# Optimization experiments

Measured on AMD Instinct MI355X. Metric: run time of the kernel, lower is better.

## Reference

```python
import jax, jax.numpy as jnp
import numpy as np

# ViT-Base config
C, H, W = 3, 224, 224
NP = 14            # n_patches per side
PS = 16            # patch size (H // NP)
IN_D = C * PS * PS # 768
D = 768            # hidden_d
NH = 12            # n_heads
DH = D // NH       # 64
L = 12             # n_blocks
MLP = 4 * D        # mlp_ratio * hidden_d
OUT = 1000         # out_d
B = 64             # batch
S = NP * NP + 1    # 197 tokens (cls + patches)
EPS = 1e-5


def _pos_embed(seq_len, d):
    # get_positional_embeddings: sin on even dims, cos on odd dims
    i = jnp.arange(seq_len, dtype=jnp.float32)[:, None]
    j = jnp.arange(d, dtype=jnp.float32)[None, :]
    angle = i / jnp.power(10000.0, (j - j % 2) / d)
    return jnp.where(j % 2 == 0, jnp.sin(angle), jnp.cos(angle))


def _ln(x, g, b):
    m = x.mean(-1, keepdims=True)
    v = ((x - m) ** 2).mean(-1, keepdims=True)
    return (x - m) * jax.lax.rsqrt(v + EPS) * g + b


def _attn(x, qkv_w, qkv_b, out_w, out_b):
    n, s, _ = x.shape
    qkv = (x @ qkv_w + qkv_b).reshape(n, s, NH, 3, DH)  # matches torch chunk layout
    q, k, v = qkv[..., 0, :], qkv[..., 1, :], qkv[..., 2, :]
    scores = jnp.einsum('bqhd,bkhd->bhqk', q, k) / (DH ** 0.5)
    w = jax.nn.softmax(scores, axis=-1)
    o = jnp.einsum('bhqk,bkhd->bqhd', w, v).reshape(n, s, D)
    return o @ out_w + out_b


def setup_inputs() -> dict:
    key = jax.random.key(0)
    ks = jax.random.split(key, 16)
    sd = 0.02
    return {
        'images': jax.random.normal(ks[0], (B, C, H, W), jnp.float32),
        'lm_w': jax.random.normal(ks[1], (IN_D, D), jnp.float32) * sd,
        'lm_b': jnp.zeros((D,), jnp.float32),
        'cls_tok': jax.random.uniform(ks[2], (1, D), jnp.float32),
        'ln1_g': jnp.ones((L, D), jnp.float32),
        'ln1_b': jnp.zeros((L, D), jnp.float32),
        'qkv_w': jax.random.normal(ks[3], (L, D, 3 * D), jnp.float32) * sd,
        'qkv_b': jnp.zeros((L, 3 * D), jnp.float32),
        'out_w': jax.random.normal(ks[4], (L, D, D), jnp.float32) * sd,
        'out_b': jnp.zeros((L, D), jnp.float32),
        'ln2_g': jnp.ones((L, D), jnp.float32),
        'ln2_b': jnp.zeros((L, D), jnp.float32),
        'mlp1_w': jax.random.normal(ks[5], (L, D, MLP), jnp.float32) * sd,
        'mlp1_b': jnp.zeros((L, MLP), jnp.float32),
        'mlp2_w': jax.random.normal(ks[6], (L, MLP, D), jnp.float32) * sd,
        'mlp2_b': jnp.zeros((L, D), jnp.float32),
        'head_w': jax.random.normal(ks[7], (D, OUT), jnp.float32) * sd,
        'head_b': jnp.zeros((OUT,), jnp.float32),
    }


def reference(images, lm_w, lm_b, cls_tok, ln1_g, ln1_b, qkv_w, qkv_b,
              out_w, out_b, ln2_g, ln2_b, mlp1_w, mlp1_b, mlp2_w, mlp2_b,
              head_w, head_b):
    n = images.shape[0]
    # patchify: (N,C,H,W) -> (N, NP*NP, C*PS*PS), per-patch flatten order (C, ph, pw)
    p = images.reshape(n, C, NP, PS, NP, PS).transpose(0, 2, 4, 1, 3, 5)
    p = p.reshape(n, NP * NP, IN_D)
    tok = p @ lm_w + lm_b                                   # (N, 196, D)
    cls = jnp.broadcast_to(cls_tok, (n, 1, D))
    x = jnp.concatenate([cls, tok], axis=1) + _pos_embed(S, D)
    for l in range(L):
        x = x + _attn(_ln(x, ln1_g[l], ln1_b[l]), qkv_w[l], qkv_b[l], out_w[l], out_b[l])
        h = _ln(x, ln2_g[l], ln2_b[l])
        x = x + (jax.nn.gelu(h @ mlp1_w[l] + mlp1_b[l], approximate=False) @ mlp2_w[l] + mlp2_b[l])
    return jax.nn.softmax(x[:, 0] @ head_w + head_b, axis=-1)
```

## Files before the change

kernel.cpp:

```cpp
#include <hip/hip_runtime.h>
#include <hip/hip_bf16.h>
#include <math.h>

#define WS_B 64
#define WS_S 197
#define WS_D 768
#define WS_NH 12
#define WS_L 12
#define WS_MLP 3072
#define WS_OUT 1000
#define WS_IND 768
#define WS_NPAT 196
#define SP 208
#define JP 224

typedef __attribute__((ext_vector_type(8))) short bf16x8;
typedef __attribute__((ext_vector_type(4))) float f32x4;

static __device__ __forceinline__ float bf2f(short s) {
    unsigned u = ((unsigned)(unsigned short)s) << 16;
    return __builtin_bit_cast(float, u);
}
static __device__ __forceinline__ short f2bf(float f) {
    unsigned u = __builtin_bit_cast(unsigned, f);
    u = (u + 0x7FFF + ((u >> 16) & 1)) >> 16;
    return (short)u;
}

static __device__ __forceinline__ int xcd_remap(int wg, int nwg) {
    int q = nwg >> 3, r = nwg & 7;
    int xcd = wg & 7, idx = wg >> 3;
    return (xcd < r ? xcd * (q + 1) : r * (q + 1) + (xcd - r) * q) + idx;
}

__global__ __launch_bounds__(256) void wconv_kernel(
    const float* __restrict__ W, short* __restrict__ Wh, int K, int N)
{
    int idx = blockIdx.x * 256 + threadIdx.x;
    int total = (K >> 3) * N;
    if (idx >= total) return;
    int n = idx % N, k8 = idx / N, k0 = k8 << 3;
    short hi[8];
#pragma unroll
    for (int j = 0; j < 8; ++j) hi[j] = f2bf(W[(size_t)(k0 + j) * N + n]);
    *(bf16x8*)(Wh + (size_t)n * K + k0) = *(bf16x8*)hi;
}

__global__ __launch_bounds__(256) void mfma_gemm(
    const short* __restrict__ A, int lda,
    const short* __restrict__ Bh,
    const float* __restrict__ bias, const float* __restrict__ res,
    float* __restrict__ outF, short* __restrict__ outH, int ldc,
    int M, int N, int K, int act)
{
    __shared__ short As[128 * 64];
    __shared__ short Bs[128 * 64];

    const int tid = threadIdx.x;
    const int w = tid >> 6, lane = tid & 63;
    const int nwg = gridDim.x * gridDim.y;
    int wg = blockIdx.y * gridDim.x + blockIdx.x;
    wg = xcd_remap(wg, nwg);
    const int bm = (wg / gridDim.x) * 128, bn = (wg % gridDim.x) * 128;
    const int wm = (w >> 1) * 64, wn = (w & 1) * 64;
    const int lr = lane & 15, lq = lane >> 4;

    f32x4 acc[4][4];
#pragma unroll
    for (int i = 0; i < 4; ++i)
#pragma unroll
        for (int j = 0; j < 4; ++j) acc[i][j] = (f32x4){0.f, 0.f, 0.f, 0.f};

    int aoff[2][4], boff[2][4];
#pragma unroll
    for (int ks = 0; ks < 2; ++ks)
#pragma unroll
        for (int f = 0; f < 4; ++f) {
            int r = wm + f * 16 + lr;
            aoff[ks][f] = r * 64 + (((ks * 4 + lq) ^ (lr & 7)) << 3);
            int rn = wn + f * 16 + lr;
            boff[ks][f] = rn * 64 + (((ks * 4 + lq) ^ (lr & 7)) << 3);
        }

    int srow[4], scs[4];
#pragma unroll
    for (int i = 0; i < 4; ++i) {
        int chunk = w * 64 + i * 256 + lane;
        int row = chunk >> 3, c = chunk & 7;
        srow[i] = row;
        scs[i] = c ^ (row & 7);
    }

    for (int k0 = 0; k0 < K; k0 += 64) {
#pragma unroll
        for (int i = 0; i < 4; ++i) {
            int ldsbase = (w * 64 + i * 256) * 8;
            int arow = bm + srow[i]; if (arow >= M) arow = M - 1;
            const short* ga = A + (size_t)arow * lda + k0 + scs[i] * 8;
            __builtin_amdgcn_global_load_lds(
                (const __attribute__((address_space(1))) void*)ga,
                (__attribute__((address_space(3))) void*)(As + ldsbase), 16, 0, 0);
            const short* gh = Bh + (size_t)(bn + srow[i]) * K + k0 + scs[i] * 8;
            __builtin_amdgcn_global_load_lds(
                (const __attribute__((address_space(1))) void*)gh,
                (__attribute__((address_space(3))) void*)(Bs + ldsbase), 16, 0, 0);
        }
        asm volatile("s_waitcnt vmcnt(0)" ::: "memory");
        __syncthreads();

#pragma unroll
        for (int ks = 0; ks < 2; ++ks) {
            bf16x8 av[4], bv[4];
#pragma unroll
            for (int f = 0; f < 4; ++f) av[f] = *(const bf16x8*)&As[aoff[ks][f]];
#pragma unroll
            for (int f = 0; f < 4; ++f) bv[f] = *(const bf16x8*)&Bs[boff[ks][f]];
#pragma unroll
            for (int fm = 0; fm < 4; ++fm)
#pragma unroll
                for (int fn = 0; fn < 4; ++fn)
                    acc[fm][fn] = __builtin_amdgcn_mfma_f32_16x16x32_bf16(
                        av[fm], bv[fn], acc[fm][fn], 0, 0, 0);
        }
        __syncthreads();
    }

#pragma unroll
    for (int fm = 0; fm < 4; ++fm)
#pragma unroll
        for (int fn = 0; fn < 4; ++fn) {
            int gc = bn + wn + fn * 16 + lr;
            float bvs = bias ? bias[gc] : 0.f;
            int grb = bm + wm + fm * 16 + lq * 4;
#pragma unroll
            for (int r = 0; r < 4; ++r) {
                int gr = grb + r;
                if (gr >= M) continue;
                float v = acc[fm][fn][r] + bvs;
                if (act == 1) v = 0.5f * v * (1.f + erff(v * 0.70710678118654752440f));
                if (res) v += res[(size_t)gr * ldc + gc];
                if (outF) outF[(size_t)gr * ldc + gc] = v;
                else      outH[(size_t)gr * ldc + gc] = f2bf(v);
            }
        }
}

__global__ __launch_bounds__(256) void attn_kernel(
    const short* __restrict__ qkv, short* __restrict__ o)
{
    __shared__ short Qs[SP * 64];
    __shared__ short Ks[SP * 64];
    __shared__ short Vt[64 * 256];
    __shared__ short Ps[4][16 * 256];

    const int bh = blockIdx.x;
    const int n = bh / WS_NH, h = bh % WS_NH;
    const short* base = qkv + (size_t)n * WS_S * 2304 + h * 192;
    const int tid = threadIdx.x;
    const int w = tid >> 6, lane = tid & 63;
    const int lr = lane & 15, lq = lane >> 4;

    const bf16x8 z8 = {0, 0, 0, 0, 0, 0, 0, 0};
    for (int i = lane; i < 512; i += 64) *(bf16x8*)&Ps[w][i * 8] = z8;

    for (int u = tid; u < SP * 8; u += 256) {
        int row = u >> 3, c = u & 7;
        int cs = c ^ (row & 7);
        bf16x8 vq = z8, vk = z8;
        if (row < WS_S) {
            const short* rp = base + (size_t)row * 2304;
            vq = *(const bf16x8*)(rp + cs * 8);
            vk = *(const bf16x8*)(rp + 64 + cs * 8);
        }
        *(bf16x8*)&Qs[row * 64 + c * 8] = vq;
        *(bf16x8*)&Ks[row * 64 + c * 8] = vk;
    }

#pragma unroll
    for (int pass = 0; pass < 7; ++pass) {
        int r = pass * 32 + (tid >> 3);
        int c = tid & 7;
        bf16x8 v = z8;
        if (r < WS_S) v = *(const bf16x8*)(base + (size_t)r * 2304 + 128 + c * 8);
#pragma unroll
        for (int e = 0; e < 8; ++e) {
            int d = c * 8 + e;
            Vt[d * 256 + ((((r >> 3)) ^ (d & 7)) << 3) + (r & 7)] = v[e];
        }
    }
    __syncthreads();

    for (int qt = w; qt < 13; qt += 4) {
        bf16x8 qv[2];
#pragma unroll
        for (int ks = 0; ks < 2; ++ks)
            qv[ks] = *(const bf16x8*)&Qs[(qt * 16 + lr) * 64 + (((ks * 4 + lq) ^ (lr & 7)) << 3)];
        f32x4 acc[13];
#pragma unroll
        for (int jt = 0; jt < 13; ++jt) acc[jt] = (f32x4){0.f, 0.f, 0.f, 0.f};
#pragma unroll
        for (int jt = 0; jt < 13; ++jt)
#pragma unroll
            for (int ks = 0; ks < 2; ++ks) {
                bf16x8 kv = *(const bf16x8*)&Ks[(jt * 16 + lr) * 64 + (((ks * 4 + lq) ^ (lr & 7)) << 3)];
                acc[jt] = __builtin_amdgcn_mfma_f32_16x16x32_bf16(kv, qv[ks], acc[jt], 0, 0, 0);
            }

        float s[13][4];
        float m = -1e30f;
#pragma unroll
        for (int jt = 0; jt < 13; ++jt)
#pragma unroll
            for (int r = 0; r < 4; ++r) {
                int j = jt * 16 + lq * 4 + r;
                float v = acc[jt][r] * 0.125f;
                s[jt][r] = v;
                if (j < WS_S) m = fmaxf(m, v);
            }
        m = fmaxf(m, __shfl_xor(m, 16));
        m = fmaxf(m, __shfl_xor(m, 32));
        float sum = 0.f;
#pragma unroll
        for (int jt = 0; jt < 13; ++jt)
#pragma unroll
            for (int r = 0; r < 4; ++r) {
                int j = jt * 16 + lq * 4 + r;
                float e = (j < WS_S) ? __expf(s[jt][r] - m) : 0.f;
                s[jt][r] = e;
                sum += e;
            }
        sum += __shfl_xor(sum, 16);
        sum += __shfl_xor(sum, 32);
        float inv = (sum > 0.f) ? 1.f / sum : 0.f;

#pragma unroll
        for (int jt = 0; jt < 13; ++jt) {
            int jb = jt * 16 + lq * 4;
            int cj = jb >> 3, e = jb & 7;
            int off = lr * 256 + ((cj ^ (lr & 7)) << 3) + e;
            unsigned p01 = (unsigned)(unsigned short)f2bf(s[jt][0] * inv) |
                           ((unsigned)(unsigned short)f2bf(s[jt][1] * inv) << 16);
            unsigned p23 = (unsigned)(unsigned short)f2bf(s[jt][2] * inv) |
                           ((unsigned)(unsigned short)f2bf(s[jt][3] * inv) << 16);
            *(unsigned*)&Ps[w][off] = p01;
            *(unsigned*)&Ps[w][off + 2] = p23;
        }
        __builtin_amdgcn_s_waitcnt(0);

        bf16x8 pa[7];
#pragma unroll
        for (int ks = 0; ks < 7; ++ks)
            pa[ks] = *(const bf16x8*)&Ps[w][lr * 256 + (((ks * 4 + lq) ^ (lr & 7)) << 3)];
#pragma unroll
        for (int dt = 0; dt < 4; ++dt) {
            f32x4 oacc = (f32x4){0.f, 0.f, 0.f, 0.f};
#pragma unroll
            for (int ks = 0; ks < 7; ++ks) {
                bf16x8 vb = *(const bf16x8*)&Vt[(dt * 16 + lr) * 256 + (((ks * 4 + lq) ^ (lr & 7)) << 3)];
                oacc = __builtin_amdgcn_mfma_f32_16x16x32_bf16(pa[ks], vb, oacc, 0, 0, 0);
            }
#pragma unroll
            for (int r = 0; r < 4; ++r) {
                int qg = qt * 16 + lq * 4 + r;
                if (qg < WS_S)
                    o[((size_t)n * WS_S + qg) * WS_D + h * 64 + dt * 16 + lr] = f2bf(oacc[r]);
            }
        }
    }
}

__global__ __launch_bounds__(256) void head_kernel(
    const float* __restrict__ x, const float* __restrict__ W,
    const float* __restrict__ bias, float* __restrict__ out)
{
    int c = blockIdx.x * 16 + (threadIdx.x & 15);
    int m = blockIdx.y * 16 + (threadIdx.x >> 4);
    if (c >= WS_OUT) return;
    const float* xr = x + (size_t)m * (WS_S * WS_D);
    float acc = bias[c];
    for (int k = 0; k < WS_D; ++k)
        acc = fmaf(xr[k], W[(size_t)k * WS_OUT + c], acc);
    out[(size_t)m * WS_OUT + c] = acc;
}

__global__ __launch_bounds__(256) void ln_kernel(
    const float* __restrict__ x, const float* __restrict__ g,
    const float* __restrict__ b, short* __restrict__ y)
{
    __shared__ float ssum[4], ssq[4];
    const int row = blockIdx.x;
    const int tid = threadIdx.x;
    const float* xr = x + (size_t)row * WS_D;
    float v0 = xr[tid], v1 = xr[tid + 256], v2 = xr[tid + 512];
    float s = v0 + v1 + v2;
    float q = v0 * v0 + v1 * v1 + v2 * v2;
#pragma unroll
    for (int off = 32; off > 0; off >>= 1) {
        s += __shfl_xor(s, off);
        q += __shfl_xor(q, off);
    }
    if ((tid & 63) == 0) { ssum[tid >> 6] = s; ssq[tid >> 6] = q; }
    __syncthreads();
    s = ssum[0] + ssum[1] + ssum[2] + ssum[3];
    q = ssq[0] + ssq[1] + ssq[2] + ssq[3];
    const float mean = s * (1.f / WS_D);
    const float var = q * (1.f / WS_D) - mean * mean;
    const float rstd = rsqrtf(var + 1e-5f);
    short* yr = y + (size_t)row * WS_D;
    yr[tid]       = f2bf((v0 - mean) * rstd * g[tid]       + b[tid]);
    yr[tid + 256] = f2bf((v1 - mean) * rstd * g[tid + 256] + b[tid + 256]);
    yr[tid + 512] = f2bf((v2 - mean) * rstd * g[tid + 512] + b[tid + 512]);
}

__global__ void pe_kernel(float* __restrict__ pe)
{
    int idx = blockIdx.x * 256 + threadIdx.x;
    if (idx >= WS_S * WS_D) return;
    int s = idx / WS_D, j = idx % WS_D;
    float expo = (float)(j & ~1) / (float)WS_D;
    float angle = (float)s * powf(10000.f, -expo);
    pe[idx] = (j & 1) ? cosf(angle) : sinf(angle);
}

__global__ void patchify_kernel(const float* __restrict__ img, short* __restrict__ p)
{
    int idx = blockIdx.x * 256 + threadIdx.x;
    const int total = WS_B * WS_NPAT * WS_IND;
    if (idx >= total) return;
    int pid = idx / WS_IND;
    int e = idx % WS_IND;
    int n = pid / WS_NPAT, patch = pid % WS_NPAT;
    int c = e >> 8, r = e & 255;
    int iy = r >> 4, ix = r & 15;
    int py = patch / 14, px = patch % 14;
    p[idx] = f2bf(img[(((size_t)n * 3 + c) * 224 + py * 16 + iy) * 224 + px * 16 + ix]);
}

__global__ void assemble_kernel(const float* __restrict__ tok, const float* __restrict__ cls,
                                const float* __restrict__ pe, float* __restrict__ x)
{
    int idx = blockIdx.x * 256 + threadIdx.x;
    const int total = WS_B * WS_S * WS_D;
    if (idx >= total) return;
    int row = idx / WS_D, d = idx % WS_D;
    int n = row / WS_S, s = row % WS_S;
    float v = (s == 0) ? cls[d] : tok[((size_t)n * WS_NPAT + (s - 1)) * WS_D + d];
    x[idx] = v + pe[s * WS_D + d];
}

__global__ __launch_bounds__(256) void softmax1000_kernel(
    const float* __restrict__ logits, float* __restrict__ out)
{
    __shared__ float rmax[4], rsum[4];
    const int row = blockIdx.x;
    const int tid = threadIdx.x;
    const float* lr = logits + (size_t)row * WS_OUT;
    float v[4];
    float mx = -INFINITY;
#pragma unroll
    for (int i = 0; i < 4; ++i) {
        int c = tid + i * 256;
        v[i] = (c < WS_OUT) ? lr[c] : -INFINITY;
        mx = fmaxf(mx, v[i]);
    }
#pragma unroll
    for (int off = 32; off > 0; off >>= 1) mx = fmaxf(mx, __shfl_xor(mx, off));
    if ((tid & 63) == 0) rmax[tid >> 6] = mx;
    __syncthreads();
    mx = fmaxf(fmaxf(rmax[0], rmax[1]), fmaxf(rmax[2], rmax[3]));
    float sum = 0.f;
#pragma unroll
    for (int i = 0; i < 4; ++i) {
        int c = tid + i * 256;
        v[i] = (c < WS_OUT) ? expf(v[i] - mx) : 0.f;
        sum += v[i];
    }
#pragma unroll
    for (int off = 32; off > 0; off >>= 1) sum += __shfl_xor(sum, off);
    if ((tid & 63) == 0) rsum[tid >> 6] = sum;
    __syncthreads();
    sum = rsum[0] + rsum[1] + rsum[2] + rsum[3];
    const float inv = 1.f / sum;
#pragma unroll
    for (int i = 0; i < 4; ++i) {
        int c = tid + i * 256;
        if (c < WS_OUT) out[(size_t)row * WS_OUT + c] = v[i] * inv;
    }
}

extern "C" void kernel_launch(void* const* d_in, const int* in_sizes, int n_in,
                              void* d_out, int out_size, void* d_ws, size_t ws_size,
                              hipStream_t stream)
{
    const float* images = (const float*)d_in[0];
    const float* lm_w   = (const float*)d_in[1];
    const float* lm_b   = (const float*)d_in[2];
    const float* cls    = (const float*)d_in[3];
    const float* ln1_g  = (const float*)d_in[4];
    const float* ln1_b  = (const float*)d_in[5];
    const float* qkv_w  = (const float*)d_in[6];
    const float* qkv_b  = (const float*)d_in[7];
    const float* out_w  = (const float*)d_in[8];
    const float* out_b  = (const float*)d_in[9];
    const float* ln2_g  = (const float*)d_in[10];
    const float* ln2_b  = (const float*)d_in[11];
    const float* mlp1_w = (const float*)d_in[12];
    const float* mlp1_b = (const float*)d_in[13];
    const float* mlp2_w = (const float*)d_in[14];
    const float* mlp2_b = (const float*)d_in[15];
    const float* head_w = (const float*)d_in[16];
    const float* head_b = (const float*)d_in[17];

    const int ROWS = WS_B * WS_S;
    char* wsb = (char*)d_ws;
    size_t off = 0;
    auto alloc = [&](size_t bytes) {
        void* p = wsb + off;
        off += (bytes + 255) & ~(size_t)255;
        return p;
    };
    float* pe     = (float*)alloc((size_t)WS_S * WS_D * 4);
    float* x      = (float*)alloc((size_t)ROWS * WS_D * 4);
    short* xh     = (short*)alloc((size_t)ROWS * WS_D * 2);
    short* qkvh   = (short*)alloc((size_t)ROWS * 2304 * 2);
    short* oh     = (short*)alloc((size_t)ROWS * WS_D * 2);
    short* hh     = (short*)alloc((size_t)ROWS * WS_MLP * 2);
    float* logits = (float*)alloc((size_t)WS_B * WS_OUT * 4);
    short* ph     = (short*)alloc((size_t)WS_B * WS_NPAT * WS_IND * 2);
    short* qWh  = (short*)alloc((size_t)WS_D * 2304 * 2);
    short* oWh  = (short*)alloc((size_t)WS_D * WS_D * 2);
    short* m1Wh = (short*)alloc((size_t)WS_D * WS_MLP * 2);
    short* m2Wh = (short*)alloc((size_t)WS_MLP * WS_D * 2);
    short* lmWh = (short*)alloc((size_t)WS_IND * WS_D * 2);
    float* tok  = (float*)hh;

    pe_kernel<<<(WS_S * WS_D + 255) / 256, 256, 0, stream>>>(pe);
    patchify_kernel<<<(WS_B * WS_NPAT * WS_IND + 255) / 256, 256, 0, stream>>>(images, ph);
    wconv_kernel<<<(WS_IND / 8 * WS_D + 255) / 256, 256, 0, stream>>>(lm_w, lmWh, WS_IND, WS_D);
    mfma_gemm<<<dim3(6, 98), 256, 0, stream>>>(
        ph, WS_IND, lmWh, lm_b, nullptr, tok, nullptr, WS_D,
        WS_B * WS_NPAT, WS_D, WS_IND, 0);
    assemble_kernel<<<(WS_B * WS_S * WS_D + 255) / 256, 256, 0, stream>>>(tok, cls, pe, x);

    for (int l = 0; l < WS_L; ++l) {
        wconv_kernel<<<(WS_D / 8 * 2304 + 255) / 256, 256, 0, stream>>>(
            qkv_w + (size_t)l * WS_D * 2304, qWh, WS_D, 2304);
        wconv_kernel<<<(WS_D / 8 * WS_D + 255) / 256, 256, 0, stream>>>(
            out_w + (size_t)l * WS_D * WS_D, oWh, WS_D, WS_D);
        wconv_kernel<<<(WS_D / 8 * WS_MLP + 255) / 256, 256, 0, stream>>>(
            mlp1_w + (size_t)l * WS_D * WS_MLP, m1Wh, WS_D, WS_MLP);
        wconv_kernel<<<(WS_MLP / 8 * WS_D + 255) / 256, 256, 0, stream>>>(
            mlp2_w + (size_t)l * WS_MLP * WS_D, m2Wh, WS_MLP, WS_D);

        ln_kernel<<<ROWS, 256, 0, stream>>>(x, ln1_g + l * WS_D, ln1_b + l * WS_D, xh);
        mfma_gemm<<<dim3(18, 99), 256, 0, stream>>>(
            xh, WS_D, qWh, qkv_b + l * 2304, nullptr, nullptr, qkvh, 2304,
            ROWS, 2304, WS_D, 0);
        attn_kernel<<<WS_B * WS_NH, 256, 0, stream>>>(qkvh, oh);
        mfma_gemm<<<dim3(6, 99), 256, 0, stream>>>(
            oh, WS_D, oWh, out_b + l * WS_D, x, x, nullptr, WS_D,
            ROWS, WS_D, WS_D, 0);
        ln_kernel<<<ROWS, 256, 0, stream>>>(x, ln2_g + l * WS_D, ln2_b + l * WS_D, xh);
        mfma_gemm<<<dim3(24, 99), 256, 0, stream>>>(
            xh, WS_D, m1Wh, mlp1_b + l * WS_MLP, nullptr, nullptr, hh, WS_MLP,
            ROWS, WS_MLP, WS_D, 1);
        mfma_gemm<<<dim3(6, 99), 256, 0, stream>>>(
            hh, WS_MLP, m2Wh, mlp2_b + l * WS_D, x, x, nullptr, WS_D,
            ROWS, WS_D, WS_MLP, 0);
    }

    head_kernel<<<dim3((WS_OUT + 15) / 16, 4), 256, 0, stream>>>(x, head_w, head_b, logits);
    softmax1000_kernel<<<WS_B, 256, 0, stream>>>(logits, (float*)d_out);
}
```

Measured before the change: 5.841 ms.

## Double-buffer GEMM LDS tiles and add 256x256 GEMM for QKV and MLP1

The existing GEMM gains double-buffered LDS staging, so the next K tile's global-to-LDS loads overlap the MFMA work on the current tile. It also raises wave priority around the MFMA block. A new 512-thread kernel with 256x256 tiles and 128 KB of LDS replaces the old GEMM for the wide QKV and MLP1 projections, to increase operand reuse. The larger tile leaves partial tiles at M=12608 and few workgroups per CU, and the single waitcnt before the barrier is now implicit, so the overlap depends on how the compiler schedules it.

New measurement: 6.698 ms. 14.7% more time.

```diff
diff --git a/kernel.cpp b/kernel.cpp
--- a/kernel.cpp
+++ b/kernel.cpp
@@ -53,8 +53,7 @@
     float* __restrict__ outF, short* __restrict__ outH, int ldc,
     int M, int N, int K, int act)
 {
-    __shared__ short As[128 * 64];
-    __shared__ short Bs[128 * 64];
+    __shared__ short lds[32768];
 
     const int tid = threadIdx.x;
     const int w = tid >> 6, lane = tid & 63;
@@ -85,48 +84,176 @@
     int srow[4], scs[4];
 #pragma unroll
     for (int i = 0; i < 4; ++i) {
-        int chunk = w * 64 + i * 256 + lane;
-        int row = chunk >> 3, c = chunk & 7;
+        int cid = i * 256 + tid;
+        int row = cid >> 3, c = cid & 7;
         srow[i] = row;
         scs[i] = c ^ (row & 7);
     }
 
-    for (int k0 = 0; k0 < K; k0 += 64) {
+    const int nt = K >> 6;
+
+    auto STAGE = [&](int kt, int slot) {
+        const int k0 = kt << 6;
+        short* Ab = &lds[slot * 8192];
+        short* Bb = &lds[16384 + slot * 8192];
 #pragma unroll
         for (int i = 0; i < 4; ++i) {
-            int ldsbase = (w * 64 + i * 256) * 8;
+            int cid = i * 256 + tid;
             int arow = bm + srow[i]; if (arow >= M) arow = M - 1;
             const short* ga = A + (size_t)arow * lda + k0 + scs[i] * 8;
             __builtin_amdgcn_global_load_lds(
                 (const __attribute__((address_space(1))) void*)ga,
-                (__attribute__((address_space(3))) void*)(As + ldsbase), 16, 0, 0);
-            const short* gh = Bh + (size_t)(bn + srow[i]) * K + k0 + scs[i] * 8;
+                (__attribute__((address_space(3))) void*)(Ab + cid * 8), 16, 0, 0);
+            const short* gb = Bh + (size_t)(bn + srow[i]) * K + k0 + scs[i] * 8;
             __builtin_amdgcn_global_load_lds(
-                (const __attribute__((address_space(1))) void*)gh,
-                (__attribute__((address_space(3))) void*)(Bs + ldsbase), 16, 0, 0);
-        }
-        asm volatile("s_waitcnt vmcnt(0)" ::: "memory");
-        __syncthreads();
-
+                (const __attribute__((address_space(1))) void*)gb,
+                (__attribute__((address_space(3))) void*)(Bb + cid * 8), 16, 0, 0);
+        }
+    };
+
+    STAGE(0, 0);
+    __syncthreads();
+
+    for (int t = 0; t < nt; ++t) {
+        if (t + 1 < nt) STAGE(t + 1, (t + 1) & 1);
+        const short* Ab = &lds[(t & 1) * 8192];
+        const short* Bb = &lds[16384 + (t & 1) * 8192];
 #pragma unroll
         for (int ks = 0; ks < 2; ++ks) {
             bf16x8 av[4], bv[4];
 #pragma unroll
-            for (int f = 0; f < 4; ++f) av[f] = *(const bf16x8*)&As[aoff[ks][f]];
-#pragma unroll
-            for (int f = 0; f < 4; ++f) bv[f] = *(const bf16x8*)&Bs[boff[ks][f]];
+            for (int f = 0; f < 4; ++f) av[f] = *(const bf16x8*)&Ab[aoff[ks][f]];
+#pragma unroll
+            for (int f = 0; f < 4; ++f) bv[f] = *(const bf16x8*)&Bb[boff[ks][f]];
+            __builtin_amdgcn_s_setprio(1);
 #pragma unroll
             for (int fm = 0; fm < 4; ++fm)
 #pragma unroll
                 for (int fn = 0; fn < 4; ++fn)
                     acc[fm][fn] = __builtin_amdgcn_mfma_f32_16x16x32_bf16(
                         av[fm], bv[fn], acc[fm][fn], 0, 0, 0);
+            __builtin_amdgcn_s_setprio(0);
         }
         __syncthreads();
     }
 
 #pragma unroll
     for (int fm = 0; fm < 4; ++fm)
+#pragma unroll
+        for (int fn = 0; fn < 4; ++fn) {
+            int gc = bn + wn + fn * 16 + lr;
+            float bvs = bias ? bias[gc] : 0.f;
+            int grb = bm + wm + fm * 16 + lq * 4;
+#pragma unroll
+            for (int r = 0; r < 4; ++r) {
+                int gr = grb + r;
+                if (gr >= M) continue;
+                float v = acc[fm][fn][r] + bvs;
+                if (act == 1) v = 0.5f * v * (1.f + erff(v * 0.70710678118654752440f));
+                if (res) v += res[(size_t)gr * ldc + gc];
+                if (outF) outF[(size_t)gr * ldc + gc] = v;
+                else      outH[(size_t)gr * ldc + gc] = f2bf(v);
+            }
+        }
+}
+
+__global__ __launch_bounds__(512) void gemm3(
+    const short* __restrict__ A, int lda,
+    const short* __restrict__ Bh,
+    const float* __restrict__ bias, const float* __restrict__ res,
+    float* __restrict__ outF, short* __restrict__ outH, int ldc,
+    int M, int N, int K, int act)
+{
+    __shared__ short lds[65536];
+
+    const int tid = threadIdx.x;
+    const int w = tid >> 6, lane = tid & 63;
+    const int nwg = gridDim.x * gridDim.y;
+    int wg = blockIdx.y * gridDim.x + blockIdx.x;
+    wg = xcd_remap(wg, nwg);
+    const int bm = (wg / gridDim.x) * 256, bn = (wg % gridDim.x) * 256;
+    const int wm = (w >> 2) * 128, wn = (w & 3) * 64;
+    const int lr = lane & 15, lq = lane >> 4;
+
+    f32x4 acc[8][4];
+#pragma unroll
+    for (int i = 0; i < 8; ++i)
+#pragma unroll
+        for (int j = 0; j < 4; ++j) acc[i][j] = (f32x4){0.f, 0.f, 0.f, 0.f};
+
+    int aoff[2][8], boff[2][4];
+#pragma unroll
+    for (int ks = 0; ks < 2; ++ks) {
+#pragma unroll
+        for (int f = 0; f < 8; ++f) {
+            int r = wm + f * 16 + lr;
+            aoff[ks][f] = r * 64 + (((ks * 4 + lq) ^ (lr & 7)) << 3);
+        }
+#pragma unroll
+        for (int f = 0; f < 4; ++f) {
+            int r = wn + f * 16 + lr;
+            boff[ks][f] = r * 64 + (((ks * 4 + lq) ^ (lr & 7)) << 3);
+        }
+    }
+
+    int srow[4], scs[4];
+#pragma unroll
+    for (int i = 0; i < 4; ++i) {
+        int cid = i * 512 + tid;
+        int row = cid >> 3, c = cid & 7;
+        srow[i] = row;
+        scs[i] = c ^ (row & 7);
+    }
+
+    const int nt = K >> 6;
+
+    auto STAGE = [&](int kt, int slot) {
+        const int k0 = kt << 6;
+        short* Ab = &lds[slot * 16384];
+        short* Bb = &lds[32768 + slot * 16384];
+#pragma unroll
+        for (int i = 0; i < 4; ++i) {
+            int cid = i * 512 + tid;
+            int arow = bm + srow[i]; if (arow >= M) arow = M - 1;
+            const short* ga = A + (size_t)arow * lda + k0 + scs[i] * 8;
+            __builtin_amdgcn_global_load_lds(
+                (const __attribute__((address_space(1))) void*)ga,
+                (__attribute__((address_space(3))) void*)(Ab + cid * 8), 16, 0, 0);
+            const short* gb = Bh + (size_t)(bn + srow[i]) * K + k0 + scs[i] * 8;
+            __builtin_amdgcn_global_load_lds(
+                (const __attribute__((address_space(1))) void*)gb,
+                (__attribute__((address_space(3))) void*)(Bb + cid * 8), 16, 0, 0);
+        }
+    };
+
+    STAGE(0, 0);
+    __syncthreads();
+
+    for (int t = 0; t < nt; ++t) {
+        if (t + 1 < nt) STAGE(t + 1, (t + 1) & 1);
+        const short* Ab = &lds[(t & 1) * 16384];
+        const short* Bb = &lds[32768 + (t & 1) * 16384];
+#pragma unroll
+        for (int ks = 0; ks < 2; ++ks) {
+            bf16x8 av[8], bv[4];
+#pragma unroll
+            for (int f = 0; f < 8; ++f) av[f] = *(const bf16x8*)&Ab[aoff[ks][f]];
+#pragma unroll
+            for (int f = 0; f < 4; ++f) bv[f] = *(const bf16x8*)&Bb[boff[ks][f]];
+            __builtin_amdgcn_s_setprio(1);
+#pragma unroll
+            for (int fm = 0; fm < 8; ++fm)
+#pragma unroll
+                for (int fn = 0; fn < 4; ++fn)
+                    acc[fm][fn] = __builtin_amdgcn_mfma_f32_16x16x32_bf16(
+                        av[fm], bv[fn], acc[fm][fn], 0, 0, 0);
+            __builtin_amdgcn_s_setprio(0);
+        }
+        __syncthreads();
+    }
+
+#pragma unroll
+    for (int fm = 0; fm < 8; ++fm)
 #pragma unroll
         for (int fn = 0; fn < 4; ++fn) {
             int gc = bn + wn + fn * 16 + lr;
@@ -453,7 +580,7 @@
             mlp2_w + (size_t)l * WS_MLP * WS_D, m2Wh, WS_MLP, WS_D);
 
         ln_kernel<<<ROWS, 256, 0, stream>>>(x, ln1_g + l * WS_D, ln1_b + l * WS_D, xh);
-        mfma_gemm<<<dim3(18, 99), 256, 0, stream>>>(
+        gemm3<<<dim3(9, 50), 512, 0, stream>>>(
             xh, WS_D, qWh, qkv_b + l * 2304, nullptr, nullptr, qkvh, 2304,
             ROWS, 2304, WS_D, 0);
         attn_kernel<<<WS_B * WS_NH, 256, 0, stream>>>(qkvh, oh);
@@ -461,7 +588,7 @@
             oh, WS_D, oWh, out_b + l * WS_D, x, x, nullptr, WS_D,
             ROWS, WS_D, WS_D, 0);
         ln_kernel<<<ROWS, 256, 0, stream>>>(x, ln2_g + l * WS_D, ln2_b + l * WS_D, xh);
-        mfma_gemm<<<dim3(24, 99), 256, 0, stream>>>(
+        gemm3<<<dim3(12, 50), 512, 0, stream>>>(
             xh, WS_D, m1Wh, mlp1_b + l * WS_MLP, nullptr, nullptr, hh, WS_MLP,
             ROWS, WS_MLP, WS_D, 1);
         mfma_gemm<<<dim3(6, 99), 256, 0, stream>>>(
```

## Double-buffer GEMM LDS tiles and batch weight conversion across layers

Applied to the files above, without the earlier changes.

The MFMA GEMM now keeps two LDS slots and prefetches the tile two steps ahead, using partial vmcnt waits and raw barriers so global-to-LDS loads overlap MFMA work. It also raises wave priority around the MFMA block. Weight conversion to bf16 moves out of the layer loop into four batched launches over all layers, with per-layer buffers. This cuts per-layer launches and exposed load latency, at the cost of more workspace and doubled LDS (64KB), which may lower occupancy.

Result: slower. 6.456 ms (+10.5%).

```diff
diff --git a/kernel.cpp b/kernel.cpp
--- a/kernel.cpp
+++ b/kernel.cpp
@@ -36,14 +36,17 @@
 __global__ __launch_bounds__(256) void wconv_kernel(
     const float* __restrict__ W, short* __restrict__ Wh, int K, int N)
 {
+    const int l = blockIdx.y;
+    const float* Wl = W + (size_t)l * K * N;
+    short* Whl = Wh + (size_t)l * N * K;
     int idx = blockIdx.x * 256 + threadIdx.x;
     int total = (K >> 3) * N;
     if (idx >= total) return;
     int n = idx % N, k8 = idx / N, k0 = k8 << 3;
     short hi[8];
 #pragma unroll
-    for (int j = 0; j < 8; ++j) hi[j] = f2bf(W[(size_t)(k0 + j) * N + n]);
-    *(bf16x8*)(Wh + (size_t)n * K + k0) = *(bf16x8*)hi;
+    for (int j = 0; j < 8; ++j) hi[j] = f2bf(Wl[(size_t)(k0 + j) * N + n]);
+    *(bf16x8*)(Whl + (size_t)n * K + k0) = *(bf16x8*)hi;
 }
 
 __global__ __launch_bounds__(256) void mfma_gemm(
@@ -53,8 +56,7 @@
     float* __restrict__ outF, short* __restrict__ outH, int ldc,
     int M, int N, int K, int act)
 {
-    __shared__ short As[128 * 64];
-    __shared__ short Bs[128 * 64];
+    __shared__ short lds[32768];
 
     const int tid = threadIdx.x;
     const int w = tid >> 6, lane = tid & 63;
@@ -85,44 +87,62 @@
     int srow[4], scs[4];
 #pragma unroll
     for (int i = 0; i < 4; ++i) {
-        int chunk = w * 64 + i * 256 + lane;
-        int row = chunk >> 3, c = chunk & 7;
+        int cid = i * 256 + tid;
+        int row = cid >> 3, c = cid & 7;
         srow[i] = row;
         scs[i] = c ^ (row & 7);
     }
 
-    for (int k0 = 0; k0 < K; k0 += 64) {
+    const int nt = K >> 6;
+
+    auto STAGE = [&](int kt, int slot) {
+        const int k0 = kt << 6;
+        short* Ab = &lds[slot * 8192];
+        short* Bb = &lds[16384 + slot * 8192];
 #pragma unroll
         for (int i = 0; i < 4; ++i) {
-            int ldsbase = (w * 64 + i * 256) * 8;
+            int cid = i * 256 + tid;
             int arow = bm + srow[i]; if (arow >= M) arow = M - 1;
             const short* ga = A + (size_t)arow * lda + k0 + scs[i] * 8;
             __builtin_amdgcn_global_load_lds(
                 (const __attribute__((address_space(1))) void*)ga,
-                (__attribute__((address_space(3))) void*)(As + ldsbase), 16, 0, 0);
-            const short* gh = Bh + (size_t)(bn + srow[i]) * K + k0 + scs[i] * 8;
+                (__attribute__((address_space(3))) void*)(Ab + cid * 8), 16, 0, 0);
+            const short* gb = Bh + (size_t)(bn + srow[i]) * K + k0 + scs[i] * 8;
             __builtin_amdgcn_global_load_lds(
-                (const __attribute__((address_space(1))) void*)gh,
-                (__attribute__((address_space(3))) void*)(Bs + ldsbase), 16, 0, 0);
-        }
-        asm volatile("s_waitcnt vmcnt(0)" ::: "memory");
-        __syncthreads();
-
+                (const __attribute__((address_space(1))) void*)gb,
+                (__attribute__((address_space(3))) void*)(Bb + cid * 8), 16, 0, 0);
+        }
+    };
+
+    STAGE(0, 0);
+    if (nt > 1) STAGE(1, 1);
+
+    for (int t = 0; t < nt; ++t) {
+        if (t + 1 < nt) asm volatile("s_waitcnt vmcnt(8)" ::: "memory");
+        else            asm volatile("s_waitcnt vmcnt(0)" ::: "memory");
+        asm volatile("s_barrier" ::: "memory");
+
+        const short* Ab = &lds[(t & 1) * 8192];
+        const short* Bb = &lds[16384 + (t & 1) * 8192];
 #pragma unroll
         for (int ks = 0; ks < 2; ++ks) {
             bf16x8 av[4], bv[4];
 #pragma unroll
-            for (int f = 0; f < 4; ++f) av[f] = *(const bf16x8*)&As[aoff[ks][f]];
-#pragma unroll
-            for (int f = 0; f < 4; ++f) bv[f] = *(const bf16x8*)&Bs[boff[ks][f]];
+            for (int f = 0; f < 4; ++f) av[f] = *(const bf16x8*)&Ab[aoff[ks][f]];
+#pragma unroll
+            for (int f = 0; f < 4; ++f) bv[f] = *(const bf16x8*)&Bb[boff[ks][f]];
+            __builtin_amdgcn_s_setprio(1);
 #pragma unroll
             for (int fm = 0; fm < 4; ++fm)
 #pragma unroll
                 for (int fn = 0; fn < 4; ++fn)
                     acc[fm][fn] = __builtin_amdgcn_mfma_f32_16x16x32_bf16(
                         av[fm], bv[fn], acc[fm][fn], 0, 0, 0);
-        }
-        __syncthreads();
+            __builtin_amdgcn_s_setprio(0);
+        }
+
+        asm volatile("s_barrier" ::: "memory");
+        if (t + 2 < nt) STAGE(t + 2, t & 1);
     }
 
 #pragma unroll
@@ -427,46 +447,42 @@
     short* hh     = (short*)alloc((size_t)ROWS * WS_MLP * 2);
     float* logits = (float*)alloc((size_t)WS_B * WS_OUT * 4);
     short* ph     = (short*)alloc((size_t)WS_B * WS_NPAT * WS_IND * 2);
-    short* qWh  = (short*)alloc((size_t)WS_D * 2304 * 2);
-    short* oWh  = (short*)alloc((size_t)WS_D * WS_D * 2);
-    short* m1Wh = (short*)alloc((size_t)WS_D * WS_MLP * 2);
-    short* m2Wh = (short*)alloc((size_t)WS_MLP * WS_D * 2);
-    short* lmWh = (short*)alloc((size_t)WS_IND * WS_D * 2);
+    short* qW_all  = (short*)alloc((size_t)WS_L * WS_D * 2304 * 2);
+    short* oW_all  = (short*)alloc((size_t)WS_L * WS_D * WS_D * 2);
+    short* m1W_all = (short*)alloc((size_t)WS_L * WS_D * WS_MLP * 2);
+    short* m2W_all = (short*)alloc((size_t)WS_L * WS_MLP * WS_D * 2);
+    short* lmWh    = (short*)alloc((size_t)WS_IND * WS_D * 2);
     float* tok  = (float*)hh;
 
     pe_kernel<<<(WS_S * WS_D + 255) / 256, 256, 0, stream>>>(pe);
     patchify_kernel<<<(WS_B * WS_NPAT * WS_IND + 255) / 256, 256, 0, stream>>>(images, ph);
-    wconv_kernel<<<(WS_IND / 8 * WS_D + 255) / 256, 256, 0, stream>>>(lm_w, lmWh, WS_IND, WS_D);
+    wconv_kernel<<<dim3((WS_IND / 8 * WS_D + 255) / 256, 1), 256, 0, stream>>>(lm_w, lmWh, WS_IND, WS_D);
+    wconv_kernel<<<dim3((WS_D / 8 * 2304 + 255) / 256, WS_L), 256, 0, stream>>>(qkv_w, qW_all, WS_D, 2304);
+    wconv_kernel<<<dim3((WS_D / 8 * WS_D + 255) / 256, WS_L), 256, 0, stream>>>(out_w, oW_all, WS_D, WS_D);
+    wconv_kernel<<<dim3((WS_D / 8 * WS_MLP + 255) / 256, WS_L), 256, 0, stream>>>(mlp1_w, m1W_all, WS_D, WS_MLP);
+    wconv_kernel<<<dim3((WS_MLP / 8 * WS_D + 255) / 256, WS_L), 256, 0, stream>>>(mlp2_w, m2W_all, WS_MLP, WS_D);
+
     mfma_gemm<<<dim3(6, 98), 256, 0, stream>>>(
         ph, WS_IND, lmWh, lm_b, nullptr, tok, nullptr, WS_D,
         WS_B * WS_NPAT, WS_D, WS_IND, 0);
     assemble_kernel<<<(WS_B * WS_S * WS_D + 255) / 256, 256, 0, stream>>>(tok, cls, pe, x);
 
     for (int l = 0; l < WS_L; ++l) {
-        wconv_kernel<<<(WS_D / 8 * 2304 + 255) / 256, 256, 0, stream>>>(
-            qkv_w + (size_t)l * WS_D * 2304, qWh, WS_D, 2304);
-        wconv_kernel<<<(WS_D / 8 * WS_D + 255) / 256, 256, 0, stream>>>(
-            out_w + (size_t)l * WS_D * WS_D, oWh, WS_D, WS_D);
-        wconv_kernel<<<(WS_D / 8 * WS_MLP + 255) / 256, 256, 0, stream>>>(
-            mlp1_w + (size_t)l * WS_D * WS_MLP, m1Wh, WS_D, WS_MLP);
-        wconv_kernel<<<(WS_MLP / 8 * WS_D + 255) / 256, 256, 0, stream>>>(
-            mlp2_w + (size_t)l * WS_MLP * WS_D, m2Wh, WS_MLP, WS_D);
-
         ln_kernel<<<ROWS, 256, 0, stream>>>(x, ln1_g + l * WS_D, ln1_b + l * WS_D, xh);
         mfma_gemm<<<dim3(18, 99), 256, 0, stream>>>(
-            xh, WS_D, qWh, qkv_b + l * 2304, nullptr, nullptr, qkvh, 2304,
-            ROWS, 2304, WS_D, 0);
+            xh, WS_D, qW_all + (size_t)l * WS_D * 2304, qkv_b + l * 2304,
+            nullptr, nullptr, qkvh, 2304, ROWS, 2304, WS_D, 0);
         attn_kernel<<<WS_B * WS_NH, 256, 0, stream>>>(qkvh, oh);
         mfma_gemm<<<dim3(6, 99), 256, 0, stream>>>(
-            oh, WS_D, oWh, out_b + l * WS_D, x, x, nullptr, WS_D,
-            ROWS, WS_D, WS_D, 0);
+            oh, WS_D, oW_all + (size_t)l * WS_D * WS_D, out_b + l * WS_D,
+            x, x, nullptr, WS_D, ROWS, WS_D, WS_D, 0);
         ln_kernel<<<ROWS, 256, 0, stream>>>(x, ln2_g + l * WS_D, ln2_b + l * WS_D, xh);
         mfma_gemm<<<dim3(24, 99), 256, 0, stream>>>(
-            xh, WS_D, m1Wh, mlp1_b + l * WS_MLP, nullptr, nullptr, hh, WS_MLP,
-            ROWS, WS_MLP, WS_D, 1);
+            xh, WS_D, m1W_all + (size_t)l * WS_D * WS_MLP, mlp1_b + l * WS_MLP,
+            nullptr, nullptr, hh, WS_MLP, ROWS, WS_MLP, WS_D, 1);
         mfma_gemm<<<dim3(6, 99), 256, 0, stream>>>(
-            hh, WS_MLP, m2Wh, mlp2_b + l * WS_D, x, x, nullptr, WS_D,
-            ROWS, WS_D, WS_MLP, 0);
+            hh, WS_MLP, m2W_all + (size_t)l * WS_MLP * WS_D, mlp2_b + l * WS_D,
+            x, x, nullptr, WS_D, ROWS, WS_D, WS_MLP, 0);
     }
 
     head_kernel<<<dim3((WS_OUT + 15) / 16, 4), 256, 0, stream>>>(x, head_w, head_b, logits);
```
